# Performance work log

Measured on AMD Instinct MI355X. Metric: run time of the kernel, lower is better.

Reference implementation:

```python
import jax, jax.numpy as jnp
import numpy as np

N = 200000   # nodes
DEG = 32     # fixed padded degree
B = 16384    # batch of target nodes
D = 128      # feature dim (app/loc/time)
H = 128      # hidden dim
L = 5        # walk length (hard-coded in original forward)


def setup_inputs() -> dict:
    key = jax.random.key(0)
    ks = jax.random.split(key, 12)
    return {
        "x_app": jax.random.normal(ks[0], (N, D), jnp.float32),
        "x_loc": jax.random.normal(ks[1], (N, D), jnp.float32),
        "x_time": jax.random.normal(ks[2], (N, H), jnp.float32),
        "neighbors": jax.random.randint(ks[3], (N, DEG), 0, N, jnp.int32),
        "edge_weight": jax.random.uniform(ks[4], (N, DEG), jnp.float32, 1e-4, 1.0),
        "target_nodes": jax.random.randint(ks[5], (B,), 0, N, jnp.int32),
        "W_app": 0.05 * jax.random.normal(ks[6], (2 * D, H), jnp.float32),
        "b_app": jnp.zeros((H,), jnp.float32),
        "W_loc": 0.05 * jax.random.normal(ks[7], (2 * D, H), jnp.float32),
        "b_loc": jnp.zeros((H,), jnp.float32),
        "W_att": 0.05 * jax.random.normal(ks[8], (D + H, 1), jnp.float32),
        "b_att": jnp.zeros((1,), jnp.float32),
    }


def _walks(neighbors, edge_weight, start, key):
    """Batched weighted random walk. start: [B] -> walk node ids [B, L+1]."""
    def step(cur, k):
        nbrs = neighbors[cur]                 # [B, DEG] gather
        w = edge_weight[cur]                  # [B, DEG]
        # multinomial(prob,1) == categorical over log-weights
        c = jax.random.categorical(k, jnp.log(w), axis=-1)   # [B]
        nxt = jnp.take_along_axis(nbrs, c[:, None], axis=1)[:, 0]
        return nxt, nxt
    _, steps = jax.lax.scan(step, start, jax.random.split(key, L))  # steps: [L, B]
    return jnp.concatenate([start[None, :], steps], axis=0).T       # [B, L+1]


def reference(x_app, x_loc, x_time, neighbors, edge_weight, target_nodes,
              W_app, b_app, W_loc, b_loc, W_att, b_att):
    kw = jax.random.key(42)
    k1, k2 = jax.random.split(kw)
    app_walk = _walks(neighbors, edge_weight, target_nodes, k1)  # [B, L+1]
    loc_walk = _walks(neighbors, edge_weight, target_nodes, k2)  # [B, L+1]

    t_app = x_app[target_nodes]                                   # [B, D]
    t_loc = x_loc[target_nodes]                                   # [B, D]

    # SameTypeAggregator: sum neighbor feats, cat with target, Linear+ReLU
    f_app = jax.nn.relu(jnp.concatenate([t_app, x_app[app_walk].sum(axis=1)], axis=-1) @ W_app + b_app)
    f_loc = jax.nn.relu(jnp.concatenate([t_loc, x_loc[loc_walk].sum(axis=1)], axis=-1) @ W_loc + b_loc)

    # CrossTypeAttention over 3 feature types
    feats = jnp.stack([f_app, f_loc, x_time[target_nodes]], axis=0)      # [3, B, H]
    tgt = jnp.broadcast_to(t_app[None], (3,) + t_app.shape)              # [3, B, D]
    combined = jnp.concatenate([tgt, feats], axis=-1)                    # [3, B, D+H]
    scores = jax.nn.softmax(combined @ W_att + b_att, axis=0)            # [3, B, 1]
    return (scores * feats).sum(axis=0)                                  # [B, H]
```

## Files before the change

kernel.cpp:

```cpp
#include <hip/hip_runtime.h>
#include <stdint.h>

#define NN 200000
#define DEG 32
#define BB 16384
#define DD 128
#define HH 128
#define BM 16

typedef __attribute__((ext_vector_type(8))) short bf16x8;
typedef __attribute__((ext_vector_type(4))) float f32x4;

struct Keys { unsigned a[5][2]; unsigned l[5][2]; };

__host__ __device__ __forceinline__ unsigned rotl32(unsigned v, int r) {
  return (v << r) | (v >> (32 - r));
}

__host__ __device__ __forceinline__ void threefry2x32(
    unsigned k0, unsigned k1, unsigned x0, unsigned x1,
    unsigned* o0, unsigned* o1) {
  unsigned ks0 = k0, ks1 = k1, ks2 = k0 ^ k1 ^ 0x1BD11BDAu;
  x0 += ks0; x1 += ks1;
#define TF_RND(r) { x0 += x1; x1 = rotl32(x1, (r)); x1 ^= x0; }
  TF_RND(13) TF_RND(15) TF_RND(26) TF_RND(6)
  x0 += ks1; x1 += ks2 + 1u;
  TF_RND(17) TF_RND(29) TF_RND(16) TF_RND(24)
  x0 += ks2; x1 += ks0 + 2u;
  TF_RND(13) TF_RND(15) TF_RND(26) TF_RND(6)
  x0 += ks0; x1 += ks1 + 3u;
  TF_RND(17) TF_RND(29) TF_RND(16) TF_RND(24)
  x0 += ks1; x1 += ks2 + 4u;
  TF_RND(13) TF_RND(15) TF_RND(26) TF_RND(6)
  x0 += ks2; x1 += ks0 + 5u;
#undef TF_RND
  *o0 = x0; *o1 = x1;
}

__device__ __forceinline__ unsigned short f2bf(float x) {
  unsigned u = __float_as_uint(x);
  unsigned r = (u + 0x7fffu + ((u >> 16) & 1u)) >> 16;
  return (unsigned short)r;
}

__global__ __launch_bounds__(256) void walk_kernel(
    const int* __restrict__ neighbors, const float* __restrict__ ew,
    const int* __restrict__ target, int* __restrict__ walks, Keys keys) {
  int lane = threadIdx.x & 63;
  int sub = lane & 31;
  int grp = (int)((blockIdx.x * 256 + threadIdx.x) >> 5);
  int wk = grp >= BB ? 1 : 0;
  int b = grp - wk * BB;

  int cur = target[b];
  if (sub == 0) walks[(size_t)grp * 6] = cur;

  const float TINY = 1.17549435e-38f;

  for (int s = 0; s < 5; ++s) {
    int nb = neighbors[(size_t)cur * DEG + sub];
    float w = ew[(size_t)cur * DEG + sub];
    unsigned j = (unsigned)b * DEG + (unsigned)sub;
    unsigned k0 = wk ? keys.l[s][0] : keys.a[s][0];
    unsigned k1 = wk ? keys.l[s][1] : keys.a[s][1];
    unsigned y0, y1;
    threefry2x32(k0, k1, 0u, j, &y0, &y1);
    unsigned bits = y0 ^ y1;
    float f = __uint_as_float((bits >> 9) | 0x3f800000u) - 1.0f;
    float u = fmaxf(TINY, f + TINY);
    float g = -logf(-logf(u));
    float v = g + logf(w);
    int idx = sub;
    #pragma unroll
    for (int off = 16; off; off >>= 1) {
      float vo = __shfl_xor(v, off);
      int io = __shfl_xor(idx, off);
      if (vo > v || (vo == v && io < idx)) { v = vo; idx = io; }
    }
    cur = __shfl(nb, (lane & 32) + idx);
    if (sub == 0) walks[(size_t)grp * 6 + s + 1] = cur;
  }
}

__global__ __launch_bounds__(256) void prep_w(
    const float* __restrict__ Wapp, const float* __restrict__ Wloc,
    unsigned short* __restrict__ Wt) {
  int blk = blockIdx.x;
  int mat = blk >> 3;
  int k0 = (blk & 7) << 5;
  const float* W = mat ? Wloc : Wapp;
  __shared__ float tile[32][129];
  int t = threadIdx.x;
  #pragma unroll
  for (int i = 0; i < 16; ++i) {
    int idx = t + (i << 8);
    int kk = idx >> 7, n = idx & 127;
    tile[kk][n] = W[((size_t)(k0 + kk) << 7) + n];
  }
  __syncthreads();
  int n = t >> 1, h = (t & 1) << 4;
  unsigned pk[8];
  #pragma unroll
  for (int j = 0; j < 8; ++j) {
    float lo = tile[h + 2 * j][n];
    float hi = tile[h + 2 * j + 1][n];
    pk[j] = (unsigned)f2bf(lo) | ((unsigned)f2bf(hi) << 16);
  }
  unsigned short* dst = Wt + ((size_t)mat << 15) + ((size_t)n << 8) + k0 + h;
  uint4 lo4; lo4.x = pk[0]; lo4.y = pk[1]; lo4.z = pk[2]; lo4.w = pk[3];
  uint4 hi4; hi4.x = pk[4]; hi4.y = pk[5]; hi4.z = pk[6]; hi4.w = pk[7];
  reinterpret_cast<uint4*>(dst)[0] = lo4;
  reinterpret_cast<uint4*>(dst)[1] = hi4;
}

__global__ __launch_bounds__(256, 4) void fuse3(
    const float* __restrict__ x_app, const float* __restrict__ x_loc,
    const float* __restrict__ x_time, const int* __restrict__ target,
    const int* __restrict__ walks, const unsigned short* __restrict__ Wt,
    const float* __restrict__ W_att, const float* __restrict__ b_att,
    const float* __restrict__ b_app, const float* __restrict__ b_loc,
    float* __restrict__ out) {
  __shared__ unsigned short sA[BM][264];
  __shared__ unsigned short sL[BM][264];
  __shared__ float attT[BM];
  __shared__ float4 sRed[4][BM];

  int tid = threadIdx.x;
  int b0 = blockIdx.x * BM;
  int hw = tid >> 5;
  int c = tid & 31;

  #pragma unroll
  for (int it = 0; it < BM / 8; ++it) {
    int row = (it << 3) + hw;
    {
      const int* wp = walks + (size_t)(b0 + row) * 6;
      int n0 = wp[0], n1 = wp[1], n2 = wp[2], n3 = wp[3], n4 = wp[4], n5 = wp[5];
      const float4 v0 = *(const float4*)&x_app[((size_t)n0 << 7) + 4 * c];
      const float4 v1 = *(const float4*)&x_app[((size_t)n1 << 7) + 4 * c];
      const float4 v2 = *(const float4*)&x_app[((size_t)n2 << 7) + 4 * c];
      const float4 v3 = *(const float4*)&x_app[((size_t)n3 << 7) + 4 * c];
      const float4 v4 = *(const float4*)&x_app[((size_t)n4 << 7) + 4 * c];
      const float4 v5 = *(const float4*)&x_app[((size_t)n5 << 7) + 4 * c];
      float sx = v0.x + v1.x + v2.x + v3.x + v4.x + v5.x;
      float sy = v0.y + v1.y + v2.y + v3.y + v4.y + v5.y;
      float sz = v0.z + v1.z + v2.z + v3.z + v4.z + v5.z;
      float sw = v0.w + v1.w + v2.w + v3.w + v4.w + v5.w;
      uint2 pt, ps;
      pt.x = (unsigned)f2bf(v0.x) | ((unsigned)f2bf(v0.y) << 16);
      pt.y = (unsigned)f2bf(v0.z) | ((unsigned)f2bf(v0.w) << 16);
      ps.x = (unsigned)f2bf(sx) | ((unsigned)f2bf(sy) << 16);
      ps.y = (unsigned)f2bf(sz) | ((unsigned)f2bf(sw) << 16);
      *(uint2*)&sA[row][4 * c] = pt;
      *(uint2*)&sA[row][128 + 4 * c] = ps;
      const float4 wa = *(const float4*)&W_att[4 * c];
      float p = v0.x * wa.x + v0.y * wa.y + v0.z * wa.z + v0.w * wa.w;
      #pragma unroll
      for (int off = 16; off; off >>= 1) p += __shfl_xor(p, off);
      if (c == 0) attT[row] = p;
    }
    {
      const int* wp = walks + (size_t)(BB + b0 + row) * 6;
      int n0 = wp[0], n1 = wp[1], n2 = wp[2], n3 = wp[3], n4 = wp[4], n5 = wp[5];
      const float4 v0 = *(const float4*)&x_loc[((size_t)n0 << 7) + 4 * c];
      const float4 v1 = *(const float4*)&x_loc[((size_t)n1 << 7) + 4 * c];
      const float4 v2 = *(const float4*)&x_loc[((size_t)n2 << 7) + 4 * c];
      const float4 v3 = *(const float4*)&x_loc[((size_t)n3 << 7) + 4 * c];
      const float4 v4 = *(const float4*)&x_loc[((size_t)n4 << 7) + 4 * c];
      const float4 v5 = *(const float4*)&x_loc[((size_t)n5 << 7) + 4 * c];
      float sx = v0.x + v1.x + v2.x + v3.x + v4.x + v5.x;
      float sy = v0.y + v1.y + v2.y + v3.y + v4.y + v5.y;
      float sz = v0.z + v1.z + v2.z + v3.z + v4.z + v5.z;
      float sw = v0.w + v1.w + v2.w + v3.w + v4.w + v5.w;
      uint2 pt, ps;
      pt.x = (unsigned)f2bf(v0.x) | ((unsigned)f2bf(v0.y) << 16);
      pt.y = (unsigned)f2bf(v0.z) | ((unsigned)f2bf(v0.w) << 16);
      ps.x = (unsigned)f2bf(sx) | ((unsigned)f2bf(sy) << 16);
      ps.y = (unsigned)f2bf(sz) | ((unsigned)f2bf(sw) << 16);
      *(uint2*)&sL[row][4 * c] = pt;
      *(uint2*)&sL[row][128 + 4 * c] = ps;
    }
  }
  __syncthreads();

  int w = tid >> 6;
  int l = tid & 63;
  int r15 = l & 15, g = l >> 4;

  f32x4 accA[2], accL[2];
  {
    bf16x8 aF[8], lF[8];
    #pragma unroll
    for (int k = 0; k < 8; ++k) {
      aF[k] = *(const bf16x8*)&sA[r15][(k << 5) + (g << 3)];
      lF[k] = *(const bf16x8*)&sL[r15][(k << 5) + (g << 3)];
    }
    #pragma unroll
    for (int n = 0; n < 2; ++n) {
      int col = ((w << 1) + n) << 4;
      f32x4 a1 = {0.f, 0.f, 0.f, 0.f}, a2 = {0.f, 0.f, 0.f, 0.f};
      #pragma unroll
      for (int k = 0; k < 8; ++k) {
        bf16x8 bA = *(const bf16x8*)&Wt[(((size_t)col + r15) << 8) + (k << 5) + (g << 3)];
        bf16x8 bL = *(const bf16x8*)&Wt[(1 << 15) + (((size_t)col + r15) << 8) + (k << 5) + (g << 3)];
        a1 = __builtin_amdgcn_mfma_f32_16x16x32_bf16(aF[k], bA, a1, 0, 0, 0);
        a2 = __builtin_amdgcn_mfma_f32_16x16x32_bf16(lF[k], bL, a2, 0, 0, 0);
      }
      accA[n] = a1;
      accL[n] = a2;
    }
  }

  float bA[2], bL[2], wv[2];
  #pragma unroll
  for (int n = 0; n < 2; ++n) {
    int col = (((w << 1) + n) << 4) + r15;
    bA[n] = b_app[col];
    bL[n] = b_loc[col];
    wv[n] = W_att[128 + col];
  }
  float batt = b_att[0];

  int trow[4];
  #pragma unroll
  for (int r = 0; r < 4; ++r) trow[r] = target[b0 + (g << 2) + r];
  float tts[2][4];
  #pragma unroll
  for (int n = 0; n < 2; ++n)
    #pragma unroll
    for (int r = 0; r < 4; ++r)
      tts[n][r] = x_time[((size_t)trow[r] << 7) + (((w << 1) + n) << 4) + r15];

  float fa[2][4], fl[2][4];
  #pragma unroll
  for (int r = 0; r < 4; ++r) {
    float dA = 0.f, dL = 0.f, dT = 0.f;
    #pragma unroll
    for (int n = 0; n < 2; ++n) {
      fa[n][r] = fmaxf(accA[n][r] + bA[n], 0.f);
      fl[n][r] = fmaxf(accL[n][r] + bL[n], 0.f);
      dA += fa[n][r] * wv[n];
      dL += fl[n][r] * wv[n];
      dT += tts[n][r] * wv[n];
    }
    #pragma unroll
    for (int off = 1; off < 16; off <<= 1) {
      dA += __shfl_xor(dA, off);
      dL += __shfl_xor(dL, off);
      dT += __shfl_xor(dT, off);
    }
    if (r15 == 0) {
      float4 q; q.x = dA; q.y = dL; q.z = dT; q.w = 0.f;
      sRed[w][(g << 2) + r] = q;
    }
  }
  __syncthreads();

  #pragma unroll
  for (int r = 0; r < 4; ++r) {
    int row = (g << 2) + r;
    float4 q0 = sRed[0][row], q1 = sRed[1][row], q2 = sRed[2][row], q3 = sRed[3][row];
    float at = attT[row] + batt;
    float s0 = at + q0.x + q1.x + q2.x + q3.x;
    float s1 = at + q0.y + q1.y + q2.y + q3.y;
    float s2 = at + q0.z + q1.z + q2.z + q3.z;
    float m = fmaxf(s0, fmaxf(s1, s2));
    float e0 = expf(s0 - m), e1 = expf(s1 - m), e2 = expf(s2 - m);
    float inv = 1.f / (e0 + e1 + e2);
    size_t grow = (size_t)(b0 + row);
    #pragma unroll
    for (int n = 0; n < 2; ++n) {
      int col = (((w << 1) + n) << 4) + r15;
      out[(grow << 7) + col] = (e0 * fa[n][r] + e1 * fl[n][r] + e2 * tts[n][r]) * inv;
    }
  }
}

extern "C" void kernel_launch(void* const* d_in, const int* in_sizes, int n_in,
                              void* d_out, int out_size, void* d_ws, size_t ws_size,
                              hipStream_t stream) {
  (void)in_sizes; (void)n_in; (void)out_size; (void)ws_size;
  const float* x_app   = (const float*)d_in[0];
  const float* x_loc   = (const float*)d_in[1];
  const float* x_time  = (const float*)d_in[2];
  const int*   neighbors = (const int*)d_in[3];
  const float* ew      = (const float*)d_in[4];
  const int*   target  = (const int*)d_in[5];
  const float* W_app   = (const float*)d_in[6];
  const float* b_app   = (const float*)d_in[7];
  const float* W_loc   = (const float*)d_in[8];
  const float* b_loc   = (const float*)d_in[9];
  const float* W_att   = (const float*)d_in[10];
  const float* b_att   = (const float*)d_in[11];
  float* out = (float*)d_out;
  int* walks = (int*)d_ws;
  unsigned short* Wt =
      (unsigned short*)((char*)d_ws + (size_t)2 * BB * 6 * sizeof(int));

  Keys keys;
  unsigned k1a, k1b, k2a, k2b;
  threefry2x32(0u, 42u, 0u, 0u, &k1a, &k1b);
  threefry2x32(0u, 42u, 0u, 1u, &k2a, &k2b);
  for (unsigned s = 0; s < 5; ++s) {
    threefry2x32(k1a, k1b, 0u, s, &keys.a[s][0], &keys.a[s][1]);
    threefry2x32(k2a, k2b, 0u, s, &keys.l[s][0], &keys.l[s][1]);
  }

  walk_kernel<<<(2 * BB * 32) / 256, 256, 0, stream>>>(neighbors, ew, target, walks, keys);
  prep_w<<<16, 256, 0, stream>>>(W_app, W_loc, Wt);
  fuse3<<<BB / BM, 256, 0, stream>>>(x_app, x_loc, x_time, target, walks, Wt,
                                     W_att, b_att, b_app, b_loc, out);
}
```

Before: 61.13 us.

## Split fused gather+GEMM kernel into separate gather and GEMM/attention kernels

The gather and walk-sum stage moves out of the fused kernel into its own kernel with one half-warp per row, 4096 blocks in all. It writes bf16 rows and the target attention term to a workspace staging buffer. The GEMM/attention kernel then loads the staged rows into shared memory, and it now runs the app and loc MFMA loops one after the other to reduce live registers. The aim is more parallelism and latency hiding for the random gathers, at the cost of an extra kernel launch and a round trip of about 16 MB of staging data through global memory.

```diff
diff --git a/kernel.cpp b/kernel.cpp
--- a/kernel.cpp
+++ b/kernel.cpp
@@ -113,73 +113,70 @@
   reinterpret_cast<uint4*>(dst)[1] = hi4;
 }
 
-__global__ __launch_bounds__(256, 4) void fuse3(
+__global__ __launch_bounds__(256, 4) void gather_kernel(
     const float* __restrict__ x_app, const float* __restrict__ x_loc,
+    const int* __restrict__ walks, const float* __restrict__ W_att,
+    unsigned short* __restrict__ stg, float* __restrict__ attT) {
+  int tid = threadIdx.x;
+  int hw = tid >> 5;
+  int c = tid & 31;
+  int gid = blockIdx.x * 8 + hw;
+  int side = gid >> 14;
+  const float* xf = side ? x_loc : x_app;
+
+  const int* wp = walks + (size_t)gid * 6;
+  int n0 = wp[0], n1 = wp[1], n2 = wp[2], n3 = wp[3], n4 = wp[4], n5 = wp[5];
+  const float4 v0 = *(const float4*)&xf[((size_t)n0 << 7) + 4 * c];
+  const float4 v1 = *(const float4*)&xf[((size_t)n1 << 7) + 4 * c];
+  const float4 v2 = *(const float4*)&xf[((size_t)n2 << 7) + 4 * c];
+  const float4 v3 = *(const float4*)&xf[((size_t)n3 << 7) + 4 * c];
+  const float4 v4 = *(const float4*)&xf[((size_t)n4 << 7) + 4 * c];
+  const float4 v5 = *(const float4*)&xf[((size_t)n5 << 7) + 4 * c];
+  float sx = v0.x + v1.x + v2.x + v3.x + v4.x + v5.x;
+  float sy = v0.y + v1.y + v2.y + v3.y + v4.y + v5.y;
+  float sz = v0.z + v1.z + v2.z + v3.z + v4.z + v5.z;
+  float sw = v0.w + v1.w + v2.w + v3.w + v4.w + v5.w;
+  uint2 pt, ps;
+  pt.x = (unsigned)f2bf(v0.x) | ((unsigned)f2bf(v0.y) << 16);
+  pt.y = (unsigned)f2bf(v0.z) | ((unsigned)f2bf(v0.w) << 16);
+  ps.x = (unsigned)f2bf(sx) | ((unsigned)f2bf(sy) << 16);
+  ps.y = (unsigned)f2bf(sz) | ((unsigned)f2bf(sw) << 16);
+  unsigned short* dst = stg + ((size_t)gid << 8);
+  *(uint2*)&dst[4 * c] = pt;
+  *(uint2*)&dst[128 + 4 * c] = ps;
+
+  if (side == 0) {
+    const float4 wa = *(const float4*)&W_att[4 * c];
+    float p = v0.x * wa.x + v0.y * wa.y + v0.z * wa.z + v0.w * wa.w;
+    #pragma unroll
+    for (int off = 16; off; off >>= 1) p += __shfl_xor(p, off);
+    if (c == 0) attT[gid] = p;
+  }
+}
+
+__global__ __launch_bounds__(256, 4) void gemm_att(
+    const unsigned short* __restrict__ stg, const float* __restrict__ attT,
     const float* __restrict__ x_time, const int* __restrict__ target,
-    const int* __restrict__ walks, const unsigned short* __restrict__ Wt,
+    const unsigned short* __restrict__ Wt,
     const float* __restrict__ W_att, const float* __restrict__ b_att,
     const float* __restrict__ b_app, const float* __restrict__ b_loc,
     float* __restrict__ out) {
   __shared__ unsigned short sA[BM][264];
   __shared__ unsigned short sL[BM][264];
-  __shared__ float attT[BM];
   __shared__ float4 sRed[4][BM];
 
   int tid = threadIdx.x;
   int b0 = blockIdx.x * BM;
-  int hw = tid >> 5;
-  int c = tid & 31;
-
-  #pragma unroll
-  for (int it = 0; it < BM / 8; ++it) {
-    int row = (it << 3) + hw;
-    {
-      const int* wp = walks + (size_t)(b0 + row) * 6;
-      int n0 = wp[0], n1 = wp[1], n2 = wp[2], n3 = wp[3], n4 = wp[4], n5 = wp[5];
-      const float4 v0 = *(const float4*)&x_app[((size_t)n0 << 7) + 4 * c];
-      const float4 v1 = *(const float4*)&x_app[((size_t)n1 << 7) + 4 * c];
-      const float4 v2 = *(const float4*)&x_app[((size_t)n2 << 7) + 4 * c];
-      const float4 v3 = *(const float4*)&x_app[((size_t)n3 << 7) + 4 * c];
-      const float4 v4 = *(const float4*)&x_app[((size_t)n4 << 7) + 4 * c];
-      const float4 v5 = *(const float4*)&x_app[((size_t)n5 << 7) + 4 * c];
-      float sx = v0.x + v1.x + v2.x + v3.x + v4.x + v5.x;
-      float sy = v0.y + v1.y + v2.y + v3.y + v4.y + v5.y;
-      float sz = v0.z + v1.z + v2.z + v3.z + v4.z + v5.z;
-      float sw = v0.w + v1.w + v2.w + v3.w + v4.w + v5.w;
-      uint2 pt, ps;
-      pt.x = (unsigned)f2bf(v0.x) | ((unsigned)f2bf(v0.y) << 16);
-      pt.y = (unsigned)f2bf(v0.z) | ((unsigned)f2bf(v0.w) << 16);
-      ps.x = (unsigned)f2bf(sx) | ((unsigned)f2bf(sy) << 16);
-      ps.y = (unsigned)f2bf(sz) | ((unsigned)f2bf(sw) << 16);
-      *(uint2*)&sA[row][4 * c] = pt;
-      *(uint2*)&sA[row][128 + 4 * c] = ps;
-      const float4 wa = *(const float4*)&W_att[4 * c];
-      float p = v0.x * wa.x + v0.y * wa.y + v0.z * wa.z + v0.w * wa.w;
-      #pragma unroll
-      for (int off = 16; off; off >>= 1) p += __shfl_xor(p, off);
-      if (c == 0) attT[row] = p;
-    }
-    {
-      const int* wp = walks + (size_t)(BB + b0 + row) * 6;
-      int n0 = wp[0], n1 = wp[1], n2 = wp[2], n3 = wp[3], n4 = wp[4], n5 = wp[5];
-      const float4 v0 = *(const float4*)&x_loc[((size_t)n0 << 7) + 4 * c];
-      const float4 v1 = *(const float4*)&x_loc[((size_t)n1 << 7) + 4 * c];
-      const float4 v2 = *(const float4*)&x_loc[((size_t)n2 << 7) + 4 * c];
-      const float4 v3 = *(const float4*)&x_loc[((size_t)n3 << 7) + 4 * c];
-      const float4 v4 = *(const float4*)&x_loc[((size_t)n4 << 7) + 4 * c];
-      const float4 v5 = *(const float4*)&x_loc[((size_t)n5 << 7) + 4 * c];
-      float sx = v0.x + v1.x + v2.x + v3.x + v4.x + v5.x;
-      float sy = v0.y + v1.y + v2.y + v3.y + v4.y + v5.y;
-      float sz = v0.z + v1.z + v2.z + v3.z + v4.z + v5.z;
-      float sw = v0.w + v1.w + v2.w + v3.w + v4.w + v5.w;
-      uint2 pt, ps;
-      pt.x = (unsigned)f2bf(v0.x) | ((unsigned)f2bf(v0.y) << 16);
-      pt.y = (unsigned)f2bf(v0.z) | ((unsigned)f2bf(v0.w) << 16);
-      ps.x = (unsigned)f2bf(sx) | ((unsigned)f2bf(sy) << 16);
-      ps.y = (unsigned)f2bf(sz) | ((unsigned)f2bf(sw) << 16);
-      *(uint2*)&sL[row][4 * c] = pt;
-      *(uint2*)&sL[row][128 + 4 * c] = ps;
-    }
+
+  int j = tid & 31;
+  int rr = tid >> 5;
+  #pragma unroll
+  for (int p = 0; p < 2; ++p) {
+    int row = (p << 3) + rr;
+    uint4 vA = *(const uint4*)&stg[(((size_t)(b0 + row)) << 8) + (j << 3)];
+    uint4 vL = *(const uint4*)&stg[(((size_t)(BB + b0 + row)) << 8) + (j << 3)];
+    *(uint4*)&sA[row][j << 3] = vA;
+    *(uint4*)&sL[row][j << 3] = vL;
   }
   __syncthreads();
 
@@ -189,25 +186,38 @@
 
   f32x4 accA[2], accL[2];
   {
-    bf16x8 aF[8], lF[8];
-    #pragma unroll
-    for (int k = 0; k < 8; ++k) {
+    bf16x8 aF[8];
+    #pragma unroll
+    for (int k = 0; k < 8; ++k)
       aF[k] = *(const bf16x8*)&sA[r15][(k << 5) + (g << 3)];
-      lF[k] = *(const bf16x8*)&sL[r15][(k << 5) + (g << 3)];
-    }
     #pragma unroll
     for (int n = 0; n < 2; ++n) {
-      int col = ((w << 1) + n) << 4;
-      f32x4 a1 = {0.f, 0.f, 0.f, 0.f}, a2 = {0.f, 0.f, 0.f, 0.f};
+      size_t colBase = ((size_t)((((w << 1) + n) << 4) + r15)) << 8;
+      f32x4 acc = {0.f, 0.f, 0.f, 0.f};
       #pragma unroll
       for (int k = 0; k < 8; ++k) {
-        bf16x8 bA = *(const bf16x8*)&Wt[(((size_t)col + r15) << 8) + (k << 5) + (g << 3)];
-        bf16x8 bL = *(const bf16x8*)&Wt[(1 << 15) + (((size_t)col + r15) << 8) + (k << 5) + (g << 3)];
-        a1 = __builtin_amdgcn_mfma_f32_16x16x32_bf16(aF[k], bA, a1, 0, 0, 0);
-        a2 = __builtin_amdgcn_mfma_f32_16x16x32_bf16(lF[k], bL, a2, 0, 0, 0);
+        bf16x8 bF = *(const bf16x8*)&Wt[colBase + (k << 5) + (g << 3)];
+        acc = __builtin_amdgcn_mfma_f32_16x16x32_bf16(aF[k], bF, acc, 0, 0, 0);
       }
-      accA[n] = a1;
-      accL[n] = a2;
+      accA[n] = acc;
+    }
+  }
+  {
+    bf16x8 lF[8];
+    #pragma unroll
+    for (int k = 0; k < 8; ++k)
+      lF[k] = *(const bf16x8*)&sL[r15][(k << 5) + (g << 3)];
+    const unsigned short* WtL = Wt + (1 << 15);
+    #pragma unroll
+    for (int n = 0; n < 2; ++n) {
+      size_t colBase = ((size_t)((((w << 1) + n) << 4) + r15)) << 8;
+      f32x4 acc = {0.f, 0.f, 0.f, 0.f};
+      #pragma unroll
+      for (int k = 0; k < 8; ++k) {
+        bf16x8 bF = *(const bf16x8*)&WtL[colBase + (k << 5) + (g << 3)];
+        acc = __builtin_amdgcn_mfma_f32_16x16x32_bf16(lF[k], bF, acc, 0, 0, 0);
+      }
+      accL[n] = acc;
     }
   }
 
@@ -260,7 +270,7 @@
   for (int r = 0; r < 4; ++r) {
     int row = (g << 2) + r;
     float4 q0 = sRed[0][row], q1 = sRed[1][row], q2 = sRed[2][row], q3 = sRed[3][row];
-    float at = attT[row] + batt;
+    float at = attT[b0 + row] + batt;
     float s0 = at + q0.x + q1.x + q2.x + q3.x;
     float s1 = at + q0.y + q1.y + q2.y + q3.y;
     float s2 = at + q0.z + q1.z + q2.z + q3.z;
@@ -293,9 +303,12 @@
   const float* W_att   = (const float*)d_in[10];
   const float* b_att   = (const float*)d_in[11];
   float* out = (float*)d_out;
-  int* walks = (int*)d_ws;
-  unsigned short* Wt =
-      (unsigned short*)((char*)d_ws + (size_t)2 * BB * 6 * sizeof(int));
+
+  char* ws = (char*)d_ws;
+  int* walks = (int*)ws;
+  unsigned short* Wt = (unsigned short*)(ws + 786432);
+  unsigned short* stg = (unsigned short*)(ws + 917504);
+  float* attT = (float*)(ws + 17694720);
 
   Keys keys;
   unsigned k1a, k1b, k2a, k2b;
@@ -308,6 +321,7 @@
 
   walk_kernel<<<(2 * BB * 32) / 256, 256, 0, stream>>>(neighbors, ew, target, walks, keys);
   prep_w<<<16, 256, 0, stream>>>(W_app, W_loc, Wt);
-  fuse3<<<BB / BM, 256, 0, stream>>>(x_app, x_loc, x_time, target, walks, Wt,
-                                     W_att, b_att, b_app, b_loc, out);
-}
+  gather_kernel<<<(2 * BB) / 8, 256, 0, stream>>>(x_app, x_loc, walks, W_att, stg, attT);
+  gemm_att<<<BB / BM, 256, 0, stream>>>(stg, attT, x_time, target, Wt,
+                                        W_att, b_att, b_app, b_loc, out);
+}
```

Result: slower. 69.41 us (+13.5%).

## Stage walk-feature gathers into LDS with direct global-to-LDS loads

Applied to the files above, without the earlier changes.

Replaces the per-thread float4 register gathers of walk node features with global_load_lds DMA copies into a 48KB shared staging buffer. Each wave loads its own 4 targets x 6 walk nodes, waits on vmcnt, then sums and converts to bf16 from LDS. The goal is to issue many more gathers at once with less register pressure. In exchange it uses much more LDS, lowers occupancy (launch bounds go from 4 to 2), and serialises the app and loc phases.

```diff
diff --git a/kernel.cpp b/kernel.cpp
--- a/kernel.cpp
+++ b/kernel.cpp
@@ -10,6 +10,7 @@
 
 typedef __attribute__((ext_vector_type(8))) short bf16x8;
 typedef __attribute__((ext_vector_type(4))) float f32x4;
+typedef __attribute__((ext_vector_type(4))) float f4;
 
 struct Keys { unsigned a[5][2]; unsigned l[5][2]; };
 
@@ -43,6 +44,12 @@
   return (unsigned short)r;
 }
 
+__device__ __forceinline__ void gload_lds16(const float* g, float* l) {
+  __builtin_amdgcn_global_load_lds(
+      (const __attribute__((address_space(1))) void*)g,
+      (__attribute__((address_space(3))) void*)l, 16, 0, 0);
+}
+
 __global__ __launch_bounds__(256) void walk_kernel(
     const int* __restrict__ neighbors, const float* __restrict__ ew,
     const int* __restrict__ target, int* __restrict__ walks, Keys keys) {
@@ -113,13 +120,14 @@
   reinterpret_cast<uint4*>(dst)[1] = hi4;
 }
 
-__global__ __launch_bounds__(256, 4) void fuse3(
+__global__ __launch_bounds__(256, 2) void fuse4(
     const float* __restrict__ x_app, const float* __restrict__ x_loc,
     const float* __restrict__ x_time, const int* __restrict__ target,
     const int* __restrict__ walks, const unsigned short* __restrict__ Wt,
     const float* __restrict__ W_att, const float* __restrict__ b_att,
     const float* __restrict__ b_app, const float* __restrict__ b_loc,
     float* __restrict__ out) {
+  __shared__ float stage[96][128];
   __shared__ unsigned short sA[BM][264];
   __shared__ unsigned short sL[BM][264];
   __shared__ float attT[BM];
@@ -127,64 +135,79 @@
 
   int tid = threadIdx.x;
   int b0 = blockIdx.x * BM;
-  int hw = tid >> 5;
-  int c = tid & 31;
-
-  #pragma unroll
-  for (int it = 0; it < BM / 8; ++it) {
-    int row = (it << 3) + hw;
-    {
-      const int* wp = walks + (size_t)(b0 + row) * 6;
-      int n0 = wp[0], n1 = wp[1], n2 = wp[2], n3 = wp[3], n4 = wp[4], n5 = wp[5];
-      const float4 v0 = *(const float4*)&x_app[((size_t)n0 << 7) + 4 * c];
-      const float4 v1 = *(const float4*)&x_app[((size_t)n1 << 7) + 4 * c];
-      const float4 v2 = *(const float4*)&x_app[((size_t)n2 << 7) + 4 * c];
-      const float4 v3 = *(const float4*)&x_app[((size_t)n3 << 7) + 4 * c];
-      const float4 v4 = *(const float4*)&x_app[((size_t)n4 << 7) + 4 * c];
-      const float4 v5 = *(const float4*)&x_app[((size_t)n5 << 7) + 4 * c];
-      float sx = v0.x + v1.x + v2.x + v3.x + v4.x + v5.x;
-      float sy = v0.y + v1.y + v2.y + v3.y + v4.y + v5.y;
-      float sz = v0.z + v1.z + v2.z + v3.z + v4.z + v5.z;
-      float sw = v0.w + v1.w + v2.w + v3.w + v4.w + v5.w;
-      uint2 pt, ps;
-      pt.x = (unsigned)f2bf(v0.x) | ((unsigned)f2bf(v0.y) << 16);
-      pt.y = (unsigned)f2bf(v0.z) | ((unsigned)f2bf(v0.w) << 16);
-      ps.x = (unsigned)f2bf(sx) | ((unsigned)f2bf(sy) << 16);
-      ps.y = (unsigned)f2bf(sz) | ((unsigned)f2bf(sw) << 16);
-      *(uint2*)&sA[row][4 * c] = pt;
-      *(uint2*)&sA[row][128 + 4 * c] = ps;
-      const float4 wa = *(const float4*)&W_att[4 * c];
-      float p = v0.x * wa.x + v0.y * wa.y + v0.z * wa.z + v0.w * wa.w;
-      #pragma unroll
-      for (int off = 16; off; off >>= 1) p += __shfl_xor(p, off);
-      if (c == 0) attT[row] = p;
-    }
-    {
-      const int* wp = walks + (size_t)(BB + b0 + row) * 6;
-      int n0 = wp[0], n1 = wp[1], n2 = wp[2], n3 = wp[3], n4 = wp[4], n5 = wp[5];
-      const float4 v0 = *(const float4*)&x_loc[((size_t)n0 << 7) + 4 * c];
-      const float4 v1 = *(const float4*)&x_loc[((size_t)n1 << 7) + 4 * c];
-      const float4 v2 = *(const float4*)&x_loc[((size_t)n2 << 7) + 4 * c];
-      const float4 v3 = *(const float4*)&x_loc[((size_t)n3 << 7) + 4 * c];
-      const float4 v4 = *(const float4*)&x_loc[((size_t)n4 << 7) + 4 * c];
-      const float4 v5 = *(const float4*)&x_loc[((size_t)n5 << 7) + 4 * c];
-      float sx = v0.x + v1.x + v2.x + v3.x + v4.x + v5.x;
-      float sy = v0.y + v1.y + v2.y + v3.y + v4.y + v5.y;
-      float sz = v0.z + v1.z + v2.z + v3.z + v4.z + v5.z;
-      float sw = v0.w + v1.w + v2.w + v3.w + v4.w + v5.w;
-      uint2 pt, ps;
-      pt.x = (unsigned)f2bf(v0.x) | ((unsigned)f2bf(v0.y) << 16);
-      pt.y = (unsigned)f2bf(v0.z) | ((unsigned)f2bf(v0.w) << 16);
-      ps.x = (unsigned)f2bf(sx) | ((unsigned)f2bf(sy) << 16);
-      ps.y = (unsigned)f2bf(sz) | ((unsigned)f2bf(sw) << 16);
-      *(uint2*)&sL[row][4 * c] = pt;
-      *(uint2*)&sL[row][128 + 4 * c] = ps;
-    }
-  }
-  __syncthreads();
-
   int w = tid >> 6;
   int l = tid & 63;
+  int h = l >> 5;
+  int c = l & 31;
+
+  int myNodeA = 0, myNodeL = 0;
+  if (l < 24) {
+    int t4 = 4 * w + l / 6, s6 = l % 6;
+    myNodeA = walks[(size_t)(b0 + t4) * 6 + s6];
+    myNodeL = walks[(size_t)(BB + b0 + t4) * 6 + s6];
+  }
+
+  #pragma unroll
+  for (int p = 0; p < 12; ++p) {
+    int node = __shfl(myNodeA, 2 * p + h);
+    gload_lds16(&x_app[((size_t)node << 7) + (c << 2)], &stage[w * 24 + 2 * p][0]);
+  }
+  asm volatile("s_waitcnt vmcnt(0)" ::: "memory");
+  __builtin_amdgcn_sched_barrier(0);
+
+  const float4 wa = *(const float4*)&W_att[4 * c];
+  #pragma unroll
+  for (int q = 0; q < 2; ++q) {
+    int j = 2 * h + q;
+    int rbase = w * 24 + j * 6;
+    f4 v0 = *(const f4*)&stage[rbase][4 * c];
+    f4 s = v0;
+    #pragma unroll
+    for (int s6 = 1; s6 < 6; ++s6) s += *(const f4*)&stage[rbase + s6][4 * c];
+    uint2 pt, ps;
+    pt.x = (unsigned)f2bf(v0.x) | ((unsigned)f2bf(v0.y) << 16);
+    pt.y = (unsigned)f2bf(v0.z) | ((unsigned)f2bf(v0.w) << 16);
+    ps.x = (unsigned)f2bf(s.x) | ((unsigned)f2bf(s.y) << 16);
+    ps.y = (unsigned)f2bf(s.z) | ((unsigned)f2bf(s.w) << 16);
+    int tj = 4 * w + j;
+    *(uint2*)&sA[tj][4 * c] = pt;
+    *(uint2*)&sA[tj][128 + 4 * c] = ps;
+    float p0 = v0.x * wa.x + v0.y * wa.y + v0.z * wa.z + v0.w * wa.w;
+    #pragma unroll
+    for (int off = 16; off; off >>= 1) p0 += __shfl_xor(p0, off);
+    if (c == 0) attT[tj] = p0;
+  }
+
+  asm volatile("s_waitcnt lgkmcnt(0)" ::: "memory");
+  __builtin_amdgcn_sched_barrier(0);
+
+  #pragma unroll
+  for (int p = 0; p < 12; ++p) {
+    int node = __shfl(myNodeL, 2 * p + h);
+    gload_lds16(&x_loc[((size_t)node << 7) + (c << 2)], &stage[w * 24 + 2 * p][0]);
+  }
+  asm volatile("s_waitcnt vmcnt(0)" ::: "memory");
+  __builtin_amdgcn_sched_barrier(0);
+
+  #pragma unroll
+  for (int q = 0; q < 2; ++q) {
+    int j = 2 * h + q;
+    int rbase = w * 24 + j * 6;
+    f4 v0 = *(const f4*)&stage[rbase][4 * c];
+    f4 s = v0;
+    #pragma unroll
+    for (int s6 = 1; s6 < 6; ++s6) s += *(const f4*)&stage[rbase + s6][4 * c];
+    uint2 pt, ps;
+    pt.x = (unsigned)f2bf(v0.x) | ((unsigned)f2bf(v0.y) << 16);
+    pt.y = (unsigned)f2bf(v0.z) | ((unsigned)f2bf(v0.w) << 16);
+    ps.x = (unsigned)f2bf(s.x) | ((unsigned)f2bf(s.y) << 16);
+    ps.y = (unsigned)f2bf(s.z) | ((unsigned)f2bf(s.w) << 16);
+    int tj = 4 * w + j;
+    *(uint2*)&sL[tj][4 * c] = pt;
+    *(uint2*)&sL[tj][128 + 4 * c] = ps;
+  }
+  __syncthreads();
+
   int r15 = l & 15, g = l >> 4;
 
   f32x4 accA[2], accL[2];
@@ -308,6 +331,6 @@
 
   walk_kernel<<<(2 * BB * 32) / 256, 256, 0, stream>>>(neighbors, ew, target, walks, keys);
   prep_w<<<16, 256, 0, stream>>>(W_app, W_loc, Wt);
-  fuse3<<<BB / BM, 256, 0, stream>>>(x_app, x_loc, x_time, target, walks, Wt,
+  fuse4<<<BB / BM, 256, 0, stream>>>(x_app, x_loc, x_time, target, walks, Wt,
                                      W_att, b_att, b_app, b_loc, out);
 }
```

Result: slower. 64.91 us (+6.2%).

## Split fused gather+GEMM kernel into separate gather and GEMM kernels via staging buffer

Applied to the files above, without the earlier changes.

The gather and neighbor-sum of walk features move out of the fused kernel into a dedicated gather6 kernel. It runs one 32-lane unit per (side, row) and writes fp32 target and sum rows plus the attention dot to a workspace staging buffer. A second gemm6 kernel reads the staged rows, converts them to bf16 in LDS and performs the MFMA GEMM and softmax. The aim is better parallelism and latency hiding for the random gathers, at the cost of an extra 32 MB write and read of staging data and an extra launch.

```diff
diff --git a/kernel.cpp b/kernel.cpp
--- a/kernel.cpp
+++ b/kernel.cpp
@@ -113,73 +113,74 @@
   reinterpret_cast<uint4*>(dst)[1] = hi4;
 }
 
-__global__ __launch_bounds__(256, 4) void fuse3(
+__global__ void gather6(
     const float* __restrict__ x_app, const float* __restrict__ x_loc,
+    const int* __restrict__ walks, const float* __restrict__ W_att,
+    float* __restrict__ stg, float* __restrict__ attT) {
+  int tid = threadIdx.x;
+  int unit = (blockIdx.x << 3) + (tid >> 5);
+  int l = tid & 31;
+  int side = unit >> 14;
+  int b = unit & (BB - 1);
+  const float* xf = side ? x_loc : x_app;
+
+  int node = 0;
+  if (l < 6) node = walks[(size_t)unit * 6 + l];
+  int n[6];
+  #pragma unroll
+  for (int s = 0; s < 6; ++s)
+    n[s] = __shfl(node, ((tid & 63) & 32) + s);
+
+  float v[4][6];
+  #pragma unroll
+  for (int kc = 0; kc < 4; ++kc)
+    #pragma unroll
+    for (int s = 0; s < 6; ++s)
+      v[kc][s] = xf[((size_t)n[s] << 7) + (kc << 5) + l];
+
+  float* row = stg + ((size_t)unit << 8);
+  float att = 0.f;
+  #pragma unroll
+  for (int kc = 0; kc < 4; ++kc) {
+    float t0 = v[kc][0];
+    float sum = ((((t0 + v[kc][1]) + v[kc][2]) + v[kc][3]) + v[kc][4]) + v[kc][5];
+    row[(kc << 5) + l] = t0;
+    row[128 + (kc << 5) + l] = sum;
+    if (side == 0) att += t0 * W_att[(kc << 5) + l];
+  }
+  if (side == 0) {
+    #pragma unroll
+    for (int off = 16; off; off >>= 1) att += __shfl_xor(att, off);
+    if (l == 0) attT[b] = att;
+  }
+}
+
+__global__ void gemm6(
+    const float* __restrict__ stg, const float* __restrict__ attT,
     const float* __restrict__ x_time, const int* __restrict__ target,
-    const int* __restrict__ walks, const unsigned short* __restrict__ Wt,
+    const unsigned short* __restrict__ Wt,
     const float* __restrict__ W_att, const float* __restrict__ b_att,
     const float* __restrict__ b_app, const float* __restrict__ b_loc,
     float* __restrict__ out) {
   __shared__ unsigned short sA[BM][264];
   __shared__ unsigned short sL[BM][264];
-  __shared__ float attT[BM];
   __shared__ float4 sRed[4][BM];
 
   int tid = threadIdx.x;
   int b0 = blockIdx.x * BM;
-  int hw = tid >> 5;
-  int c = tid & 31;
-
-  #pragma unroll
-  for (int it = 0; it < BM / 8; ++it) {
-    int row = (it << 3) + hw;
-    {
-      const int* wp = walks + (size_t)(b0 + row) * 6;
-      int n0 = wp[0], n1 = wp[1], n2 = wp[2], n3 = wp[3], n4 = wp[4], n5 = wp[5];
-      const float4 v0 = *(const float4*)&x_app[((size_t)n0 << 7) + 4 * c];
-      const float4 v1 = *(const float4*)&x_app[((size_t)n1 << 7) + 4 * c];
-      const float4 v2 = *(const float4*)&x_app[((size_t)n2 << 7) + 4 * c];
-      const float4 v3 = *(const float4*)&x_app[((size_t)n3 << 7) + 4 * c];
-      const float4 v4 = *(const float4*)&x_app[((size_t)n4 << 7) + 4 * c];
-      const float4 v5 = *(const float4*)&x_app[((size_t)n5 << 7) + 4 * c];
-      float sx = v0.x + v1.x + v2.x + v3.x + v4.x + v5.x;
-      float sy = v0.y + v1.y + v2.y + v3.y + v4.y + v5.y;
-      float sz = v0.z + v1.z + v2.z + v3.z + v4.z + v5.z;
-      float sw = v0.w + v1.w + v2.w + v3.w + v4.w + v5.w;
-      uint2 pt, ps;
-      pt.x = (unsigned)f2bf(v0.x) | ((unsigned)f2bf(v0.y) << 16);
-      pt.y = (unsigned)f2bf(v0.z) | ((unsigned)f2bf(v0.w) << 16);
-      ps.x = (unsigned)f2bf(sx) | ((unsigned)f2bf(sy) << 16);
-      ps.y = (unsigned)f2bf(sz) | ((unsigned)f2bf(sw) << 16);
-      *(uint2*)&sA[row][4 * c] = pt;
-      *(uint2*)&sA[row][128 + 4 * c] = ps;
-      const float4 wa = *(const float4*)&W_att[4 * c];
-      float p = v0.x * wa.x + v0.y * wa.y + v0.z * wa.z + v0.w * wa.w;
-      #pragma unroll
-      for (int off = 16; off; off >>= 1) p += __shfl_xor(p, off);
-      if (c == 0) attT[row] = p;
-    }
-    {
-      const int* wp = walks + (size_t)(BB + b0 + row) * 6;
-      int n0 = wp[0], n1 = wp[1], n2 = wp[2], n3 = wp[3], n4 = wp[4], n5 = wp[5];
-      const float4 v0 = *(const float4*)&x_loc[((size_t)n0 << 7) + 4 * c];
-      const float4 v1 = *(const float4*)&x_loc[((size_t)n1 << 7) + 4 * c];
-      const float4 v2 = *(const float4*)&x_loc[((size_t)n2 << 7) + 4 * c];
-      const float4 v3 = *(const float4*)&x_loc[((size_t)n3 << 7) + 4 * c];
-      const float4 v4 = *(const float4*)&x_loc[((size_t)n4 << 7) + 4 * c];
-      const float4 v5 = *(const float4*)&x_loc[((size_t)n5 << 7) + 4 * c];
-      float sx = v0.x + v1.x + v2.x + v3.x + v4.x + v5.x;
-      float sy = v0.y + v1.y + v2.y + v3.y + v4.y + v5.y;
-      float sz = v0.z + v1.z + v2.z + v3.z + v4.z + v5.z;
-      float sw = v0.w + v1.w + v2.w + v3.w + v4.w + v5.w;
-      uint2 pt, ps;
-      pt.x = (unsigned)f2bf(v0.x) | ((unsigned)f2bf(v0.y) << 16);
-      pt.y = (unsigned)f2bf(v0.z) | ((unsigned)f2bf(v0.w) << 16);
-      ps.x = (unsigned)f2bf(sx) | ((unsigned)f2bf(sy) << 16);
-      ps.y = (unsigned)f2bf(sz) | ((unsigned)f2bf(sw) << 16);
-      *(uint2*)&sL[row][4 * c] = pt;
-      *(uint2*)&sL[row][128 + 4 * c] = ps;
-    }
+
+  #pragma unroll
+  for (int p = 0; p < 8; ++p) {
+    int idx = (p << 8) + tid;
+    int side = idx >> 10;
+    int row = (idx >> 6) & 15;
+    int ch = idx & 63;
+    const float4 vv = *(const float4*)&stg[(((size_t)(side * BB + b0 + row)) << 8) + (ch << 2)];
+    uint2 pk;
+    pk.x = (unsigned)f2bf(vv.x) | ((unsigned)f2bf(vv.y) << 16);
+    pk.y = (unsigned)f2bf(vv.z) | ((unsigned)f2bf(vv.w) << 16);
+    if (side == 0) *(uint2*)&sA[row][ch << 2] = pk;
+    else           *(uint2*)&sL[row][ch << 2] = pk;
   }
   __syncthreads();
 
@@ -260,7 +261,7 @@
   for (int r = 0; r < 4; ++r) {
     int row = (g << 2) + r;
     float4 q0 = sRed[0][row], q1 = sRed[1][row], q2 = sRed[2][row], q3 = sRed[3][row];
-    float at = attT[row] + batt;
+    float at = attT[b0 + row] + batt;
     float s0 = at + q0.x + q1.x + q2.x + q3.x;
     float s1 = at + q0.y + q1.y + q2.y + q3.y;
     float s2 = at + q0.z + q1.z + q2.z + q3.z;
@@ -293,9 +294,12 @@
   const float* W_att   = (const float*)d_in[10];
   const float* b_att   = (const float*)d_in[11];
   float* out = (float*)d_out;
-  int* walks = (int*)d_ws;
-  unsigned short* Wt =
-      (unsigned short*)((char*)d_ws + (size_t)2 * BB * 6 * sizeof(int));
+
+  char* ws = (char*)d_ws;
+  int* walks = (int*)ws;
+  unsigned short* Wt = (unsigned short*)(ws + 786432);
+  float* stg = (float*)(ws + 917504);
+  float* attT = (float*)(ws + 34471936);
 
   Keys keys;
   unsigned k1a, k1b, k2a, k2b;
@@ -308,6 +312,7 @@
 
   walk_kernel<<<(2 * BB * 32) / 256, 256, 0, stream>>>(neighbors, ew, target, walks, keys);
   prep_w<<<16, 256, 0, stream>>>(W_app, W_loc, Wt);
-  fuse3<<<BB / BM, 256, 0, stream>>>(x_app, x_loc, x_time, target, walks, Wt,
+  gather6<<<(2 * BB) / 8, 256, 0, stream>>>(x_app, x_loc, walks, W_att, stg, attT);
+  gemm6<<<BB / BM, 256, 0, stream>>>(stg, attT, x_time, target, Wt,
                                      W_att, b_att, b_app, b_loc, out);
 }
```

New measurement: 74.48 us. +21.8%, slower.
